# Optimization experiments

Measured on AMD Instinct MI355X. Metric: run time of the kernel, lower is better.

## Reference

```python
import jax, jax.numpy as jnp
import numpy as np

DT = 0.01        # base_dt from __init__
DT_SCALE = 1.0   # forward default


def setup_inputs() -> dict:
    key = jax.random.key(0)
    k1, k2, k3, k4, k5 = jax.random.split(key, 5)
    B, D, R = 4096, 512, 128
    x = jax.random.normal(k1, (B, D), dtype=jnp.float32)
    v = jax.random.normal(k2, (B, D), dtype=jnp.float32)
    force = jax.random.normal(k3, (B, D), dtype=jnp.float32)
    U = jax.random.normal(k4, (D, R), dtype=jnp.float32) * (1.0 / np.sqrt(D))
    W = jax.random.normal(k5, (R, D), dtype=jnp.float32) * (1.0 / np.sqrt(R))
    return {"x": x, "v": v, "force": force, "U": U, "W": W, "steps": 8}


def reference(x, v, force, U, W, steps):
    dt = DT * DT_SCALE
    # Dormand-Prince (DP5) tableau
    a21 = 1/5
    a31, a32 = 3/40, 9/40
    a41, a42, a43 = 44/45, -56/15, 32/9
    a51, a52, a53, a54 = 19372/6561, -25360/2187, 64448/6561, -212/729
    a61, a62, a63, a64, a65 = 9017/3168, -355/33, 46732/5247, 49/176, -5103/18656
    b1, b3, b4, b5, b6 = 35/384, 500/1113, 125/192, -2187/6784, 11/84

    def dynamics(tx, tv):
        # low-rank Christoffel: gamma(v, x) = ((v @ U) * (x @ U)) @ W
        acc = -jnp.einsum('br,rd->bd', (tv @ U) * (tx @ U), W)
        return acc + force

    def step(carry, _):
        cx, cv = carry
        k1x = cv
        k1v = dynamics(cx, cv)
        x2 = cx + dt * (a21 * k1x); v2 = cv + dt * (a21 * k1v)
        k2x = v2; k2v = dynamics(x2, v2)
        x3 = cx + dt * (a31 * k1x + a32 * k2x)
        v3 = cv + dt * (a31 * k1v + a32 * k2v)
        k3x = v3; k3v = dynamics(x3, v3)
        x4 = cx + dt * (a41 * k1x + a42 * k2x + a43 * k3x)
        v4 = cv + dt * (a41 * k1v + a42 * k2v + a43 * k3v)
        k4x = v4; k4v = dynamics(x4, v4)
        x5 = cx + dt * (a51 * k1x + a52 * k2x + a53 * k3x + a54 * k4x)
        v5 = cv + dt * (a51 * k1v + a52 * k2v + a53 * k3v + a54 * k4v)
        k5x = v5; k5v = dynamics(x5, v5)
        x6 = cx + dt * (a61 * k1x + a62 * k2x + a63 * k3x + a64 * k4x + a65 * k5x)
        v6 = cv + dt * (a61 * k1v + a62 * k2v + a63 * k3v + a64 * k4v + a65 * k5v)
        k6x = v6; k6v = dynamics(x6, v6)
        nx = cx + dt * (b1 * k1x + b3 * k3x + b4 * k4x + b5 * k5x + b6 * k6x)
        nv = cv + dt * (b1 * k1v + b3 * k3v + b4 * k4v + b5 * k5v + b6 * k6v)
        return (nx, nv), None

    (fx, fv), _ = jax.lax.scan(step, (x, v), None, length=steps)
    return fx, fv
```

## Files before the change

kernel.cpp:

```cpp
#include <hip/hip_runtime.h>


typedef _Float16 v8h __attribute__((ext_vector_type(8)));
typedef float v4f __attribute__((ext_vector_type(4)));
typedef unsigned short u16;
typedef unsigned int u32;

#define MFMAH __builtin_amdgcn_mfma_f32_16x16x32_f16
#define INV2048 4.8828125e-4f
#define INV256  0.00390625f
#define SSTR 144

__device__ __forceinline__ float swap8(float x){
  return __int_as_float(
    __builtin_amdgcn_mov_dpp(__float_as_int(x), 0x128, 0xf, 0xf, true));
}

struct Tab {
  double a[7][7]; double b[7]; double A[7]; double XC[7][7]; double XF[7]; double cxc[7];
};
static constexpr Tab make_tab() {
  Tab t{};
  t.a[2][1]=1.0/5;
  t.a[3][1]=3.0/40;       t.a[3][2]=9.0/40;
  t.a[4][1]=44.0/45;      t.a[4][2]=-56.0/15;      t.a[4][3]=32.0/9;
  t.a[5][1]=19372.0/6561; t.a[5][2]=-25360.0/2187; t.a[5][3]=64448.0/6561; t.a[5][4]=-212.0/729;
  t.a[6][1]=9017.0/3168;  t.a[6][2]=-355.0/33;     t.a[6][3]=46732.0/5247; t.a[6][4]=49.0/176; t.a[6][5]=-5103.0/18656;
  t.b[1]=35.0/384; t.b[2]=0.0; t.b[3]=500.0/1113; t.b[4]=125.0/192; t.b[5]=-2187.0/6784; t.b[6]=11.0/84;
  for (int i=1;i<=6;++i){ double s=0; for(int j=1;j<i;++j) s+=t.a[i][j]; t.A[i]=s; }
  for (int i=1;i<=6;++i) for(int l=1;l<i;++l){ double s=0; for(int j=l+1;j<i;++j) s+=t.a[i][j]*t.a[j][l]; t.XC[i][l]=s; }
  for (int i=1;i<=6;++i){ double s=0; for(int j=1;j<i;++j) s+=t.a[i][j]*t.A[j]; t.XF[i]=s; }
  for (int j=1;j<=6;++j){ double s=0; for (int i=j+1;i<=6;++i) s+=t.b[i]*t.a[i][j]; t.cxc[j]=s; }
  return t;
}
static constexpr Tab TB = make_tab();

__device__ __forceinline__ int decode_steps(const void* p){
  int v = *(const int*)p;
  if (v >= 1 && v <= 512) return v;
  float f = *(const float*)p;
  if (f >= 1.f && f <= 512.f) return (int)f;
  return 8;
}
__device__ __forceinline__ void split2s(float x, _Float16& h, _Float16& l){
  h = (_Float16)x;
  l = (_Float16)((x - (float)h) * 2048.0f);
}

#define WS_GH 0
#define WS_GL 16384
#define WS_UH 32768
#define WS_UL 98304
#define WS_WH 163840
#define WS_WL 229376

__global__ __launch_bounds__(512) void k_prep(const float* __restrict__ Ug,
                                              const float* __restrict__ Wg,
                                              _Float16* __restrict__ ws){
  const int tid = threadIdx.x;
  if (blockIdx.x >= 8) {
    int t = (blockIdx.x - 8)*512 + tid;
    if (t < 65536) {
      int r = t >> 7, c = t & 127;
      _Float16 h, l; split2s(Ug[t]*256.f, h, l);
      int kb=r>>5, q2=(r>>3)&3, j=r&7, n2=c>>4, cl=c&15;
      int slot = ((n2*16+kb)*64 + q2*16+cl)*8 + j;
      ws[WS_UH + slot] = h; ws[WS_UL + slot] = l;
    } else {
      int idx = t - 65536;
      int r = idx >> 9, c = idx & 511;
      _Float16 h, l; split2s(Wg[idx]*256.f, h, l);
      int kb=r>>5, q2=(r>>3)&3, j=r&7, n2=c>>4, cl=c&15;
      int slot = ((n2*4+kb)*64 + q2*16+cl)*8 + j;
      ws[WS_WH + slot] = h; ws[WS_WL + slot] = l;
    }
  } else {
    const int b = blockIdx.x;
    const int ww = tid >> 6, lane = tid & 63, q = lane >> 4, c16 = lane & 15;
    const int nb = ww;
    v4f aH = {0,0,0,0}, aC0 = {0,0,0,0}, aC1 = {0,0,0,0};
    #pragma unroll
    for (int kb = 0; kb < 16; ++kb) {
      const float* wp = Wg + (b*16 + c16)*512 + kb*32 + q*8;
      float4 w0 = *(const float4*)wp;
      float4 w1 = *(const float4*)(wp + 4);
      float wv[8] = {w0.x,w0.y,w0.z,w0.w, w1.x,w1.y,w1.z,w1.w};
      v8h Ah, Al, Bh, Bl;
      #pragma unroll
      for (int j = 0; j < 8; ++j) {
        _Float16 h, l; split2s(-wv[j], h, l);
        Ah[j] = h; Al[j] = l;
        float uv = Ug[(kb*32 + q*8 + j)*128 + nb*16 + c16] * 256.f;
        split2s(uv, h, l);
        Bh[j] = h; Bl[j] = l;
      }
      aH = MFMAH(Ah, Bh, aH, 0,0,0);
      if (kb & 1) {
        aC1 = MFMAH(Ah, Bl, aC1, 0,0,0);
        aC1 = MFMAH(Al, Bh, aC1, 0,0,0);
      } else {
        aC0 = MFMAH(Ah, Bl, aC0, 0,0,0);
        aC0 = MFMAH(Al, Bh, aC0, 0,0,0);
      }
    }
    #pragma unroll
    for (int r = 0; r < 4; ++r) {
      float g = aH[r] + (aC0[r] + aC1[r])*INV2048;
      _Float16 h, l; split2s(g, h, l);
      int m = b*16 + 4*q + r, n = nb*16 + c16;
      int slot = (((n>>4)*4 + (m>>5))*64 + ((m>>3)&3)*16 + (n&15))*8 + (m&7);
      ws[WS_GH + slot] = h; ws[WS_GL + slot] = l;
    }
  }
}

#define ARENA 49920

__global__ __launch_bounds__(512,4) void dp5_main(
    const float* __restrict__ xg, const float* __restrict__ vg,
    const float* __restrict__ fg, const void* stepsp,
    const _Float16* __restrict__ ws, float* __restrict__ outg)
{
  __shared__ __align__(16) char arena[ARENA];
  _Float16* base = (_Float16*)arena;
  const _Float16* uH = ws + WS_UH;
  const _Float16* uL = ws + WS_UL;
  const _Float16* wH = ws + WS_WH;
  const _Float16* wL = ws + WS_WL;

  const int tid  = threadIdx.x;
  const int ww   = tid >> 6;
  const int lane = tid & 63;
  const int q    = lane >> 4;
  const int c16  = lane & 15;
  const int nb   = ww;
  const int kcol = nb*16 + c16;
  const int srcl = (q>>1)*16 + c16;
  const bool odd = (q & 1);
  const int rb   = blockIdx.x * 8;
  const int S    = decode_steps(stepsp);
  const float dt = 0.01f;
  const int  brow = c16 & 7;
  const bool hiC  = (c16 >= 8);
  const int  kc0  = nb*16 + 4*q + (hiC ? 2 : 0);

  v8h Gh[4], Gl[4];
  #pragma unroll
  for (int kb = 0; kb < 4; ++kb) {
    int off = ((nb*4 + kb)*64 + lane)*8;
    Gh[kb] = *(const v8h*)(ws + WS_GH + off);
    Gl[kb] = *(const v8h*)(ws + WS_GL + off);
  }

  _Float16* tH = base;
  _Float16* tL = base + 12480;
  const int r16 = tid >> 5, c0 = (tid & 31)*16;
  float xU0[2], vU0[2], fU0[2];
  {
    {
      const float* sp = (r16 < 8) ? (xg + (rb + r16)*512) : (vg + (rb + r16 - 8)*512);
      sp += c0;
      float4 g0 = *(const float4*)(sp);
      float4 g1 = *(const float4*)(sp + 4);
      float4 g2 = *(const float4*)(sp + 8);
      float4 g3 = *(const float4*)(sp + 12);
      float vals[16] = {g0.x,g0.y,g0.z,g0.w, g1.x,g1.y,g1.z,g1.w,
                        g2.x,g2.y,g2.z,g2.w, g3.x,g3.y,g3.z,g3.w};
      v8h vh0, vh1, vl0, vl1;
      #pragma unroll
      for (int j = 0; j < 8; ++j) {
        _Float16 h, l;
        split2s(vals[j], h, l);     vh0[j] = h; vl0[j] = l;
        split2s(vals[8+j], h, l);   vh1[j] = h; vl1[j] = l;
      }
      int o = r16*520 + c0;
      *(v8h*)(tH + o) = vh0; *(v8h*)(tH + o + 8) = vh1;
      *(v8h*)(tL + o) = vl0; *(v8h*)(tL + o + 8) = vl1;
    }
    if (r16 < 8) {
      const float* sp = fg + (rb + r16)*512 + c0;
      float4 g0 = *(const float4*)(sp);
      float4 g1 = *(const float4*)(sp + 4);
      float4 g2 = *(const float4*)(sp + 8);
      float4 g3 = *(const float4*)(sp + 12);
      float vals[16] = {g0.x,g0.y,g0.z,g0.w, g1.x,g1.y,g1.z,g1.w,
                        g2.x,g2.y,g2.z,g2.w, g3.x,g3.y,g3.z,g3.w};
      v8h vh0, vh1, vl0, vl1;
      #pragma unroll
      for (int j = 0; j < 8; ++j) {
        _Float16 h, l;
        split2s(vals[j], h, l);     vh0[j] = h; vl0[j] = l;
        split2s(vals[8+j], h, l);   vh1[j] = h; vl1[j] = l;
      }
      int o = (16 + r16)*520 + c0;
      *(v8h*)(tH + o) = vh0; *(v8h*)(tH + o + 8) = vh1;
      *(v8h*)(tL + o) = vl0; *(v8h*)(tL + o + 8) = vl1;
    }
    __syncthreads();

    v4f aH0={0,0,0,0}, aH1={0,0,0,0}, aC0={0,0,0,0}, aC1={0,0,0,0};
    v4f bH0={0,0,0,0}, bH1={0,0,0,0}, bC0={0,0,0,0}, bC1={0,0,0,0};
    const int arow1 = (c16 < 8) ? (16 + c16) : c16;
    #pragma unroll
    for (int kb = 0; kb < 16; ++kb) {
      int ao0 = c16*520 + kb*32 + q*8;
      int ao1 = arow1*520 + kb*32 + q*8;
      v8h Ah0 = *(const v8h*)(tH + ao0);
      v8h Al0 = *(const v8h*)(tL + ao0);
      v8h Ah1 = *(const v8h*)(tH + ao1);
      v8h Al1 = *(const v8h*)(tL + ao1);
      int bo = ((nb*16 + kb)*64 + lane)*8;
      v8h Bh = *(const v8h*)(uH + bo);
      v8h Bl = *(const v8h*)(uL + bo);
      if (kb & 1) {
        aH1 = MFMAH(Ah0, Bh, aH1, 0,0,0);
        aC1 = MFMAH(Ah0, Bl, aC1, 0,0,0);
        aC1 = MFMAH(Al0, Bh, aC1, 0,0,0);
        bH1 = MFMAH(Ah1, Bh, bH1, 0,0,0);
        bC1 = MFMAH(Ah1, Bl, bC1, 0,0,0);
        bC1 = MFMAH(Al1, Bh, bC1, 0,0,0);
      } else {
        aH0 = MFMAH(Ah0, Bh, aH0, 0,0,0);
        aC0 = MFMAH(Ah0, Bl, aC0, 0,0,0);
        aC0 = MFMAH(Al0, Bh, aC0, 0,0,0);
        bH0 = MFMAH(Ah1, Bh, bH0, 0,0,0);
        bC0 = MFMAH(Ah1, Bl, bC0, 0,0,0);
        bC0 = MFMAH(Al1, Bh, bC0, 0,0,0);
      }
    }
    float at0 = ((aH0[0]+aH1[0]) + (aC0[0]+aC1[0])*INV2048)*INV256;
    float at1 = ((aH0[1]+aH1[1]) + (aC0[1]+aC1[1])*INV2048)*INV256;
    float at2 = ((aH0[2]+aH1[2]) + (aC0[2]+aC1[2])*INV2048)*INV256;
    float at3 = ((aH0[3]+aH1[3]) + (aC0[3]+aC1[3])*INV2048)*INV256;
    float bt0 = ((bH0[0]+bH1[0]) + (bC0[0]+bC1[0])*INV2048)*INV256;
    float bt1 = ((bH0[1]+bH1[1]) + (bC0[1]+bC1[1])*INV2048)*INV256;
    float bt2 = ((bH0[2]+bH1[2]) + (bC0[2]+bC1[2])*INV2048)*INV256;
    float bt3 = ((bH0[3]+bH1[3]) + (bC0[3]+bC1[3])*INV2048)*INV256;
    {
      float sx0=__shfl(at0,srcl,64), sx1=__shfl(at1,srcl,64);
      float sx2=__shfl(at2,srcl,64), sx3=__shfl(at3,srcl,64);
      xU0[0] = odd ? sx2 : sx0; xU0[1] = odd ? sx3 : sx1;
      int srclv = srcl + 32;
      float sv0=__shfl(at0,srclv,64), sv1=__shfl(at1,srclv,64);
      float sv2=__shfl(at2,srclv,64), sv3=__shfl(at3,srclv,64);
      vU0[0] = odd ? sv2 : sv0; vU0[1] = odd ? sv3 : sv1;
    }
    {
      float sf0=__shfl(bt0,srcl,64), sf1=__shfl(bt1,srcl,64);
      float sf2=__shfl(bt2,srcl,64), sf3=__shfl(bt3,srcl,64);
      fU0[0] = odd ? sf2 : sf0; fU0[1] = odd ? sf3 : sf1;
    }
    __syncthreads();
  }

  float cxU2[2], cvU2[2], fU2[2];
  {
    float* T = (float*)arena;
    #pragma unroll
    for (int p2 = 0; p2 < 3; ++p2) {
      float i0 = (p2==0) ? xU0[0] : (p2==1) ? vU0[0] : fU0[0];
      float i1 = (p2==0) ? xU0[1] : (p2==1) ? vU0[1] : fU0[1];
      T[(2*q + 0)*132 + kcol] = i0;
      T[(2*q + 1)*132 + kcol] = i1;
      __syncthreads();
      float2 t2 = *(const float2*)(T + brow*132 + kc0);
      float* o = (p2==0) ? cxU2 : (p2==1) ? cvU2 : fU2;
      o[0] = t2.x; o[1] = t2.y;
      __syncthreads();
    }
  }

  float kU6[6][2], Rr2[2], QXa2[2];
  #pragma unroll
  for (int j = 0; j < 2; ++j) {
    Rr2[j] = 0.f; QXa2[j] = 0.f;
    #pragma unroll
    for (int l = 0; l < 6; ++l) kU6[l][j] = 0.f;
  }

  int pb = 0;
  for (int s = 0; s < S; ++s) {
    float accX[2], accV[2], Pbs[2], Pxcs[2];
    #pragma unroll
    for (int j = 0; j < 2; ++j) { accX[j]=0.f; accV[j]=0.f; Pbs[j]=0.f; Pxcs[j]=0.f; }

    #pragma unroll
    for (int i = 1; i <= 6; ++i) {
      _Float16* bT = base + (pb ? 2304 : 0);
      const float dtA   = dt*(float)TB.A[i];
      const float dt2XF = dt*dt*(float)TB.XF[i];
      const float bi    = (float)TB.b[i];
      const float ci    = (float)TB.cxc[i];
      {
        union { _Float16 h[2]; u32 u; } ph, pl;
        #pragma unroll
        for (int j2 = 0; j2 < 2; ++j2) {
          float vv = cvU2[j2] + dtA*fU2[j2];
          float xx = cxU2[j2] + dtA*cvU2[j2] + dt2XF*fU2[j2];
          #pragma unroll
          for (int l = 1; l < i; ++l) {
            vv += (dt*(float)TB.a[i][l]) * kU6[l-1][j2];
            xx += (dt*dt*(float)TB.XC[i][l]) * kU6[l-1][j2];
          }
          float p = vv*xx;
          Pbs[j2] += bi*p; Pxcs[j2] += ci*p;
          _Float16 h, l2; split2s(p, h, l2);
          ph.h[j2] = h; pl.h[j2] = l2;
        }
        *(u32*)(bT + brow*SSTR + kc0)       = ph.u;
        *(u32*)(bT + (8+brow)*SSTR + kc0)   = pl.u;
      }
      __syncthreads();
      const _Float16* bp = bT + c16*SSTR + q*8;
      v8h B0 = *(const v8h*)(bp);
      v8h B1 = *(const v8h*)(bp + 32);
      v8h B2 = *(const v8h*)(bp + 64);
      v8h B3 = *(const v8h*)(bp + 96);
      v4f C1 = {0,0,0,0}, C2 = {0,0,0,0};
      C1 = MFMAH(Gh[0], B0, C1, 0,0,0);  C2 = MFMAH(Gl[0], B0, C2, 0,0,0);
      C1 = MFMAH(Gh[1], B1, C1, 0,0,0);  C2 = MFMAH(Gl[1], B1, C2, 0,0,0);
      C1 = MFMAH(Gh[2], B2, C1, 0,0,0);  C2 = MFMAH(Gl[2], B2, C2, 0,0,0);
      C1 = MFMAH(Gh[3], B3, C1, 0,0,0);  C2 = MFMAH(Gl[3], B3, C2, 0,0,0);
      float kv[4];
      #pragma unroll
      for (int r = 0; r < 4; ++r) {
        float oth = swap8(C1[r]);
        kv[r] = (C1[r] + (oth + C2[r])*INV2048)*INV256;
      }
      float k2 = swap8(kv[2]);
      float k3 = swap8(kv[3]);
      float kva = hiC ? k2 : kv[0];
      float kvb = hiC ? k3 : kv[1];
      kU6[i-1][0] = kva; kU6[i-1][1] = kvb;
      accX[0] += ci*kva; accV[0] += bi*kva;
      accX[1] += ci*kvb; accV[1] += bi*kvb;
      pb ^= 1;
    }

    #pragma unroll
    for (int j = 0; j < 2; ++j) {
      float nx = cxU2[j] + dt*cvU2[j] + dt*dt*(accX[j] + 0.5f*fU2[j]);
      cvU2[j] += dt*(accV[j] + fU2[j]);
      cxU2[j]  = nx;
      QXa2[j] += Rr2[j] + Pxcs[j];
      Rr2[j]  += Pbs[j];
    }
  }

  __syncthreads();
  _Float16* RQh = base;
  _Float16* RQl = base + 2176;
  {
    union { _Float16 h[2]; u32 u; } t1, t2, t3, t4;
    #pragma unroll
    for (int j2 = 0; j2 < 2; ++j2) {
      _Float16 h, l;
      split2s(Rr2[j2], h, l);  t1.h[j2] = h; t2.h[j2] = l;
      split2s(QXa2[j2], h, l); t3.h[j2] = h; t4.h[j2] = l;
    }
    *(u32*)(RQh + brow*136 + kc0)     = t1.u;
    *(u32*)(RQl + brow*136 + kc0)     = t2.u;
    *(u32*)(RQh + (8+brow)*136 + kc0) = t3.u;
    *(u32*)(RQl + (8+brow)*136 + kc0) = t4.u;
  }
  __syncthreads();

  float* axs = (float*)(arena + 9216);
  float* abs_ = (float*)(arena + 25600);

  #pragma unroll
  for (int cbi = 0; cbi < 4; ++cbi) {
    int cb = nb*4 + cbi;
    v4f aH={0,0,0,0}, aC0={0,0,0,0}, aC1={0,0,0,0};
    #pragma unroll
    for (int kb = 0; kb < 4; ++kb) {
      int bo = ((cb*4 + kb)*64 + lane)*8;
      v8h Bh = *(const v8h*)(wH + bo);
      v8h Bl = *(const v8h*)(wL + bo);
      int ao = c16*136 + kb*32 + q*8;
      v8h Ah = *(const v8h*)(RQh + ao);
      v8h Al = *(const v8h*)(RQl + ao);
      aH = MFMAH(Ah, Bh, aH, 0,0,0);
      if (kb & 1) {
        aC1 = MFMAH(Ah, Bl, aC1, 0,0,0);
        aC1 = MFMAH(Al, Bh, aC1, 0,0,0);
      } else {
        aC0 = MFMAH(Ah, Bl, aC0, 0,0,0);
        aC0 = MFMAH(Al, Bh, aC0, 0,0,0);
      }
    }
    float r0 = (aH[0] + (aC0[0]+aC1[0])*INV2048)*INV256;
    float r1 = (aH[1] + (aC0[1]+aC1[1])*INV2048)*INV256;
    float r2 = (aH[2] + (aC0[2]+aC1[2])*INV2048)*INV256;
    float r3 = (aH[3] + (aC0[3]+aC1[3])*INV2048)*INV256;
    float o0 = __shfl_xor(r0, 32, 64);
    float o1 = __shfl_xor(r1, 32, 64);
    float o2 = __shfl_xor(r2, 32, 64);
    float o3 = __shfl_xor(r3, 32, 64);
    if (q < 2) {
      float abv[4] = {r0, r1, r2, r3};
      float axv[4] = {o0, o1, o2, o3};
      #pragma unroll
      for (int i4 = 0; i4 < 4; ++i4) {
        int lrow = 4*q + i4;
        int lcol = cb*16 + c16;
        axs[lrow*512 + lcol]  = axv[i4];
        abs_[lrow*512 + lcol] = abv[i4];
      }
    }
  }
  __syncthreads();

  const float Sdt = (float)S * dt;
  #pragma unroll
  for (int half = 0; half < 2; ++half) {
    int flat = half*2048 + tid*4;
    int row  = flat >> 9;
    int col  = flat & 511;
    int go   = (rb + row)*512 + col;
    float4 xv = *(const float4*)(xg + go);
    float4 vv = *(const float4*)(vg + go);
    float4 fv = *(const float4*)(fg + go);
    float4 axf = *(const float4*)(axs + flat);
    float4 abf = *(const float4*)(abs_ + flat);
    float4 o1, o2;
    o1.x = xv.x + Sdt*vv.x + 0.5f*Sdt*Sdt*fv.x - dt*dt*axf.x;
    o1.y = xv.y + Sdt*vv.y + 0.5f*Sdt*Sdt*fv.y - dt*dt*axf.y;
    o1.z = xv.z + Sdt*vv.z + 0.5f*Sdt*Sdt*fv.z - dt*dt*axf.z;
    o1.w = xv.w + Sdt*vv.w + 0.5f*Sdt*Sdt*fv.w - dt*dt*axf.w;
    o2.x = vv.x + Sdt*fv.x - dt*abf.x;
    o2.y = vv.y + Sdt*fv.y - dt*abf.y;
    o2.z = vv.z + Sdt*fv.z - dt*abf.z;
    o2.w = vv.w + Sdt*fv.w - dt*abf.w;
    *(float4*)(outg + go) = o1;
    *(float4*)(outg + 2097152 + go) = o2;
  }
}

extern "C" void kernel_launch(void* const* d_in, const int* in_sizes, int n_in,
                              void* d_out, int out_size, void* d_ws, size_t ws_size,
                              hipStream_t stream) {
  const float* x = (const float*)d_in[0];
  const float* v = (const float*)d_in[1];
  const float* f = (const float*)d_in[2];
  const float* U = (const float*)d_in[3];
  const float* W = (const float*)d_in[4];
  _Float16* ws = (_Float16*)d_ws;

  k_prep<<<dim3(264), dim3(512), 0, stream>>>(U, W, ws);
  dp5_main<<<dim3(512), dim3(512), 0, stream>>>(
      x, v, f, d_in[5], ws, (float*)d_out);
}
```

Before: 136.4 us.

## Process two 8-row batches per block to interleave independent MFMA chains

Each block now handles 16 rows as two independent 8-row groups, A and B. Their per-stage phase-1 writes, MFMA chains and k-value extraction are interleaved so the two groups hide each other's latency and share the G fragments and barriers. The grid is halved and launch bounds are relaxed to 2 blocks per CU, which allows more registers but lowers occupancy. The projection and epilogue run twice per block. The k-value extraction is also reordered so the swaps apply to the selected lanes.

```diff
diff --git a/kernel.cpp b/kernel.cpp
--- a/kernel.cpp
+++ b/kernel.cpp
@@ -116,7 +116,7 @@
 
 #define ARENA 49920
 
-__global__ __launch_bounds__(512,4) void dp5_main(
+__global__ __launch_bounds__(512,2) void dp5_main(
     const float* __restrict__ xg, const float* __restrict__ vg,
     const float* __restrict__ fg, const void* stepsp,
     const _Float16* __restrict__ ws, float* __restrict__ outg)
@@ -137,26 +137,20 @@
   const int kcol = nb*16 + c16;
   const int srcl = (q>>1)*16 + c16;
   const bool odd = (q & 1);
-  const int rb   = blockIdx.x * 8;
+  const int rbA  = blockIdx.x * 16;
+  const int rbB  = rbA + 8;
   const int S    = decode_steps(stepsp);
   const float dt = 0.01f;
   const int  brow = c16 & 7;
   const bool hiC  = (c16 >= 8);
   const int  kc0  = nb*16 + 4*q + (hiC ? 2 : 0);
 
-  v8h Gh[4], Gl[4];
-  #pragma unroll
-  for (int kb = 0; kb < 4; ++kb) {
-    int off = ((nb*4 + kb)*64 + lane)*8;
-    Gh[kb] = *(const v8h*)(ws + WS_GH + off);
-    Gl[kb] = *(const v8h*)(ws + WS_GL + off);
-  }
-
-  _Float16* tH = base;
-  _Float16* tL = base + 12480;
   const int r16 = tid >> 5, c0 = (tid & 31)*16;
-  float xU0[2], vU0[2], fU0[2];
-  {
+
+  auto projection = [&](int rb, float cxU2[2], float cvU2[2], float fU2[2]) {
+    _Float16* tH = base;
+    _Float16* tL = base + 12480;
+    float xU0[2], vU0[2], fU0[2];
     {
       const float* sp = (r16 < 8) ? (xg + (rb + r16)*512) : (vg + (rb + r16 - 8)*512);
       sp += c0;
@@ -236,25 +230,24 @@
     float bt1 = ((bH0[1]+bH1[1]) + (bC0[1]+bC1[1])*INV2048)*INV256;
     float bt2 = ((bH0[2]+bH1[2]) + (bC0[2]+bC1[2])*INV2048)*INV256;
     float bt3 = ((bH0[3]+bH1[3]) + (bC0[3]+bC1[3])*INV2048)*INV256;
+    float xU0a, xU0b, vU0a, vU0b, fU0a, fU0b;
     {
       float sx0=__shfl(at0,srcl,64), sx1=__shfl(at1,srcl,64);
       float sx2=__shfl(at2,srcl,64), sx3=__shfl(at3,srcl,64);
-      xU0[0] = odd ? sx2 : sx0; xU0[1] = odd ? sx3 : sx1;
+      xU0a = odd ? sx2 : sx0; xU0b = odd ? sx3 : sx1;
       int srclv = srcl + 32;
       float sv0=__shfl(at0,srclv,64), sv1=__shfl(at1,srclv,64);
       float sv2=__shfl(at2,srclv,64), sv3=__shfl(at3,srclv,64);
-      vU0[0] = odd ? sv2 : sv0; vU0[1] = odd ? sv3 : sv1;
+      vU0a = odd ? sv2 : sv0; vU0b = odd ? sv3 : sv1;
     }
     {
       float sf0=__shfl(bt0,srcl,64), sf1=__shfl(bt1,srcl,64);
       float sf2=__shfl(bt2,srcl,64), sf3=__shfl(bt3,srcl,64);
-      fU0[0] = odd ? sf2 : sf0; fU0[1] = odd ? sf3 : sf1;
-    }
+      fU0a = odd ? sf2 : sf0; fU0b = odd ? sf3 : sf1;
+    }
+    xU0[0]=xU0a; xU0[1]=xU0b; vU0[0]=vU0a; vU0[1]=vU0b; fU0[0]=fU0a; fU0[1]=fU0b;
     __syncthreads();
-  }
-
-  float cxU2[2], cvU2[2], fU2[2];
-  {
+
     float* T = (float*)arena;
     #pragma unroll
     for (int p2 = 0; p2 < 3; ++p2) {
@@ -268,39 +261,59 @@
       o[0] = t2.x; o[1] = t2.y;
       __syncthreads();
     }
+  };
+
+  float cxA[2], cvA[2], fA[2], cxB[2], cvB[2], fB[2];
+  projection(rbA, cxA, cvA, fA);
+  projection(rbB, cxB, cvB, fB);
+
+  v8h Gh[4], Gl[4];
+  #pragma unroll
+  for (int kb = 0; kb < 4; ++kb) {
+    int off = ((nb*4 + kb)*64 + lane)*8;
+    Gh[kb] = *(const v8h*)(ws + WS_GH + off);
+    Gl[kb] = *(const v8h*)(ws + WS_GL + off);
   }
 
-  float kU6[6][2], Rr2[2], QXa2[2];
+  float kUA[6][2], kUB[6][2], RrA[2], RrB[2], QXA[2], QXB[2];
   #pragma unroll
   for (int j = 0; j < 2; ++j) {
-    Rr2[j] = 0.f; QXa2[j] = 0.f;
-    #pragma unroll
-    for (int l = 0; l < 6; ++l) kU6[l][j] = 0.f;
+    RrA[j]=0.f; RrB[j]=0.f; QXA[j]=0.f; QXB[j]=0.f;
+    #pragma unroll
+    for (int l = 0; l < 6; ++l) { kUA[l][j]=0.f; kUB[l][j]=0.f; }
   }
 
   int pb = 0;
   for (int s = 0; s < S; ++s) {
-    float accX[2], accV[2], Pbs[2], Pxcs[2];
-    #pragma unroll
-    for (int j = 0; j < 2; ++j) { accX[j]=0.f; accV[j]=0.f; Pbs[j]=0.f; Pxcs[j]=0.f; }
+    float accXA[2], accVA[2], PbsA[2], PxcsA[2];
+    float accXB[2], accVB[2], PbsB[2], PxcsB[2];
+    #pragma unroll
+    for (int j = 0; j < 2; ++j) {
+      accXA[j]=0.f; accVA[j]=0.f; PbsA[j]=0.f; PxcsA[j]=0.f;
+      accXB[j]=0.f; accVB[j]=0.f; PbsB[j]=0.f; PxcsB[j]=0.f;
+    }
 
     #pragma unroll
     for (int i = 1; i <= 6; ++i) {
-      _Float16* bT = base + (pb ? 2304 : 0);
+      _Float16* bTA = base + (pb ? 2304 : 0);
+      _Float16* bTB = base + 4608 + (pb ? 2304 : 0);
       const float dtA   = dt*(float)TB.A[i];
       const float dt2XF = dt*dt*(float)TB.XF[i];
       const float bi    = (float)TB.b[i];
       const float ci    = (float)TB.cxc[i];
-      {
+
+      auto phase1 = [&](_Float16* bT, const float cx[2], const float cv[2],
+                        const float ff[2], const float (*kU)[2],
+                        float Pbs[2], float Pxcs[2]) {
         union { _Float16 h[2]; u32 u; } ph, pl;
         #pragma unroll
         for (int j2 = 0; j2 < 2; ++j2) {
-          float vv = cvU2[j2] + dtA*fU2[j2];
-          float xx = cxU2[j2] + dtA*cvU2[j2] + dt2XF*fU2[j2];
+          float vv = cv[j2] + dtA*ff[j2];
+          float xx = cx[j2] + dtA*cv[j2] + dt2XF*ff[j2];
           #pragma unroll
           for (int l = 1; l < i; ++l) {
-            vv += (dt*(float)TB.a[i][l]) * kU6[l-1][j2];
-            xx += (dt*dt*(float)TB.XC[i][l]) * kU6[l-1][j2];
+            vv += (dt*(float)TB.a[i][l]) * kU[l-1][j2];
+            xx += (dt*dt*(float)TB.XC[i][l]) * kU[l-1][j2];
           }
           float p = vv*xx;
           Pbs[j2] += bi*p; Pxcs[j2] += ci*p;
@@ -309,132 +322,171 @@
         }
         *(u32*)(bT + brow*SSTR + kc0)       = ph.u;
         *(u32*)(bT + (8+brow)*SSTR + kc0)   = pl.u;
-      }
+      };
+      phase1(bTA, cxA, cvA, fA, kUA, PbsA, PxcsA);
+      phase1(bTB, cxB, cvB, fB, kUB, PbsB, PxcsB);
       __syncthreads();
-      const _Float16* bp = bT + c16*SSTR + q*8;
-      v8h B0 = *(const v8h*)(bp);
-      v8h B1 = *(const v8h*)(bp + 32);
-      v8h B2 = *(const v8h*)(bp + 64);
-      v8h B3 = *(const v8h*)(bp + 96);
-      v4f C1 = {0,0,0,0}, C2 = {0,0,0,0};
-      C1 = MFMAH(Gh[0], B0, C1, 0,0,0);  C2 = MFMAH(Gl[0], B0, C2, 0,0,0);
-      C1 = MFMAH(Gh[1], B1, C1, 0,0,0);  C2 = MFMAH(Gl[1], B1, C2, 0,0,0);
-      C1 = MFMAH(Gh[2], B2, C1, 0,0,0);  C2 = MFMAH(Gl[2], B2, C2, 0,0,0);
-      C1 = MFMAH(Gh[3], B3, C1, 0,0,0);  C2 = MFMAH(Gl[3], B3, C2, 0,0,0);
-      float kv[4];
+
+      const _Float16* bpA = bTA + c16*SSTR + q*8;
+      const _Float16* bpB = bTB + c16*SSTR + q*8;
+      v8h A0 = *(const v8h*)(bpA);
+      v8h A1 = *(const v8h*)(bpA + 32);
+      v8h A2 = *(const v8h*)(bpA + 64);
+      v8h A3 = *(const v8h*)(bpA + 96);
+      v8h Bb0 = *(const v8h*)(bpB);
+      v8h Bb1 = *(const v8h*)(bpB + 32);
+      v8h Bb2 = *(const v8h*)(bpB + 64);
+      v8h Bb3 = *(const v8h*)(bpB + 96);
+      v4f C1 = {0,0,0,0}, C2 = {0,0,0,0}, D1 = {0,0,0,0}, D2 = {0,0,0,0};
+      C1 = MFMAH(Gh[0], A0,  C1, 0,0,0);  D1 = MFMAH(Gh[0], Bb0, D1, 0,0,0);
+      C2 = MFMAH(Gl[0], A0,  C2, 0,0,0);  D2 = MFMAH(Gl[0], Bb0, D2, 0,0,0);
+      C1 = MFMAH(Gh[1], A1,  C1, 0,0,0);  D1 = MFMAH(Gh[1], Bb1, D1, 0,0,0);
+      C2 = MFMAH(Gl[1], A1,  C2, 0,0,0);  D2 = MFMAH(Gl[1], Bb1, D2, 0,0,0);
+      C1 = MFMAH(Gh[2], A2,  C1, 0,0,0);  D1 = MFMAH(Gh[2], Bb2, D1, 0,0,0);
+      C2 = MFMAH(Gl[2], A2,  C2, 0,0,0);  D2 = MFMAH(Gl[2], Bb2, D2, 0,0,0);
+      C1 = MFMAH(Gh[3], A3,  C1, 0,0,0);  D1 = MFMAH(Gh[3], Bb3, D1, 0,0,0);
+      C2 = MFMAH(Gl[3], A3,  C2, 0,0,0);  D2 = MFMAH(Gl[3], Bb3, D2, 0,0,0);
+
+      {
+        float sa0 = swap8(C1[0]), sa2 = swap8(C1[2]), sc2 = swap8(C2[2]);
+        float sb1 = swap8(C1[1]), sb3 = swap8(C1[3]), sd3 = swap8(C2[3]);
+        float m_a = hiC ? sa2   : C1[0];
+        float n_a = hiC ? C1[2] : sa0;
+        float c_a = hiC ? sc2   : C2[0];
+        float m_b = hiC ? sb3   : C1[1];
+        float n_b = hiC ? C1[3] : sb1;
+        float c_b = hiC ? sd3   : C2[1];
+        float kva = (m_a + (n_a + c_a)*INV2048)*INV256;
+        float kvb = (m_b + (n_b + c_b)*INV2048)*INV256;
+        kUA[i-1][0] = kva; kUA[i-1][1] = kvb;
+        accXA[0] += ci*kva; accVA[0] += bi*kva;
+        accXA[1] += ci*kvb; accVA[1] += bi*kvb;
+      }
+      {
+        float sa0 = swap8(D1[0]), sa2 = swap8(D1[2]), sc2 = swap8(D2[2]);
+        float sb1 = swap8(D1[1]), sb3 = swap8(D1[3]), sd3 = swap8(D2[3]);
+        float m_a = hiC ? sa2   : D1[0];
+        float n_a = hiC ? D1[2] : sa0;
+        float c_a = hiC ? sc2   : D2[0];
+        float m_b = hiC ? sb3   : D1[1];
+        float n_b = hiC ? D1[3] : sb1;
+        float c_b = hiC ? sd3   : D2[1];
+        float kva = (m_a + (n_a + c_a)*INV2048)*INV256;
+        float kvb = (m_b + (n_b + c_b)*INV2048)*INV256;
+        kUB[i-1][0] = kva; kUB[i-1][1] = kvb;
+        accXB[0] += ci*kva; accVB[0] += bi*kva;
+        accXB[1] += ci*kvb; accVB[1] += bi*kvb;
+      }
+      pb ^= 1;
+    }
+
+    #pragma unroll
+    for (int j = 0; j < 2; ++j) {
+      float nxA = cxA[j] + dt*cvA[j] + dt*dt*(accXA[j] + 0.5f*fA[j]);
+      cvA[j] += dt*(accVA[j] + fA[j]);
+      cxA[j]  = nxA;
+      QXA[j] += RrA[j] + PxcsA[j];
+      RrA[j] += PbsA[j];
+      float nxB = cxB[j] + dt*cvB[j] + dt*dt*(accXB[j] + 0.5f*fB[j]);
+      cvB[j] += dt*(accVB[j] + fB[j]);
+      cxB[j]  = nxB;
+      QXB[j] += RrB[j] + PxcsB[j];
+      RrB[j] += PbsB[j];
+    }
+  }
+
+  const float Sdt = (float)S * dt;
+  auto epilogue = [&](int rb, const float Rr2[2], const float QXa2[2]) {
+    __syncthreads();
+    _Float16* RQh = base;
+    _Float16* RQl = base + 2176;
+    {
+      union { _Float16 h[2]; u32 u; } t1, t2, t3, t4;
       #pragma unroll
-      for (int r = 0; r < 4; ++r) {
-        float oth = swap8(C1[r]);
-        kv[r] = (C1[r] + (oth + C2[r])*INV2048)*INV256;
-      }
-      float k2 = swap8(kv[2]);
-      float k3 = swap8(kv[3]);
-      float kva = hiC ? k2 : kv[0];
-      float kvb = hiC ? k3 : kv[1];
-      kU6[i-1][0] = kva; kU6[i-1][1] = kvb;
-      accX[0] += ci*kva; accV[0] += bi*kva;
-      accX[1] += ci*kvb; accV[1] += bi*kvb;
-      pb ^= 1;
-    }
-
-    #pragma unroll
-    for (int j = 0; j < 2; ++j) {
-      float nx = cxU2[j] + dt*cvU2[j] + dt*dt*(accX[j] + 0.5f*fU2[j]);
-      cvU2[j] += dt*(accV[j] + fU2[j]);
-      cxU2[j]  = nx;
-      QXa2[j] += Rr2[j] + Pxcs[j];
-      Rr2[j]  += Pbs[j];
-    }
-  }
-
-  __syncthreads();
-  _Float16* RQh = base;
-  _Float16* RQl = base + 2176;
-  {
-    union { _Float16 h[2]; u32 u; } t1, t2, t3, t4;
-    #pragma unroll
-    for (int j2 = 0; j2 < 2; ++j2) {
-      _Float16 h, l;
-      split2s(Rr2[j2], h, l);  t1.h[j2] = h; t2.h[j2] = l;
-      split2s(QXa2[j2], h, l); t3.h[j2] = h; t4.h[j2] = l;
-    }
-    *(u32*)(RQh + brow*136 + kc0)     = t1.u;
-    *(u32*)(RQl + brow*136 + kc0)     = t2.u;
-    *(u32*)(RQh + (8+brow)*136 + kc0) = t3.u;
-    *(u32*)(RQl + (8+brow)*136 + kc0) = t4.u;
-  }
-  __syncthreads();
-
-  float* axs = (float*)(arena + 9216);
-  float* abs_ = (float*)(arena + 25600);
-
-  #pragma unroll
-  for (int cbi = 0; cbi < 4; ++cbi) {
-    int cb = nb*4 + cbi;
-    v4f aH={0,0,0,0}, aC0={0,0,0,0}, aC1={0,0,0,0};
-    #pragma unroll
-    for (int kb = 0; kb < 4; ++kb) {
-      int bo = ((cb*4 + kb)*64 + lane)*8;
-      v8h Bh = *(const v8h*)(wH + bo);
-      v8h Bl = *(const v8h*)(wL + bo);
-      int ao = c16*136 + kb*32 + q*8;
-      v8h Ah = *(const v8h*)(RQh + ao);
-      v8h Al = *(const v8h*)(RQl + ao);
-      aH = MFMAH(Ah, Bh, aH, 0,0,0);
-      if (kb & 1) {
-        aC1 = MFMAH(Ah, Bl, aC1, 0,0,0);
-        aC1 = MFMAH(Al, Bh, aC1, 0,0,0);
-      } else {
-        aC0 = MFMAH(Ah, Bl, aC0, 0,0,0);
-        aC0 = MFMAH(Al, Bh, aC0, 0,0,0);
-      }
-    }
-    float r0 = (aH[0] + (aC0[0]+aC1[0])*INV2048)*INV256;
-    float r1 = (aH[1] + (aC0[1]+aC1[1])*INV2048)*INV256;
-    float r2 = (aH[2] + (aC0[2]+aC1[2])*INV2048)*INV256;
-    float r3 = (aH[3] + (aC0[3]+aC1[3])*INV2048)*INV256;
-    float o0 = __shfl_xor(r0, 32, 64);
-    float o1 = __shfl_xor(r1, 32, 64);
-    float o2 = __shfl_xor(r2, 32, 64);
-    float o3 = __shfl_xor(r3, 32, 64);
-    if (q < 2) {
-      float abv[4] = {r0, r1, r2, r3};
-      float axv[4] = {o0, o1, o2, o3};
+      for (int j2 = 0; j2 < 2; ++j2) {
+        _Float16 h, l;
+        split2s(Rr2[j2], h, l);  t1.h[j2] = h; t2.h[j2] = l;
+        split2s(QXa2[j2], h, l); t3.h[j2] = h; t4.h[j2] = l;
+      }
+      *(u32*)(RQh + brow*136 + kc0)     = t1.u;
+      *(u32*)(RQl + brow*136 + kc0)     = t2.u;
+      *(u32*)(RQh + (8+brow)*136 + kc0) = t3.u;
+      *(u32*)(RQl + (8+brow)*136 + kc0) = t4.u;
+    }
+    __syncthreads();
+
+    float* axs  = (float*)(arena + 9216);
+    float* abs_ = (float*)(arena + 25600);
+
+    #pragma unroll
+    for (int cbi = 0; cbi < 4; ++cbi) {
+      int cb = nb*4 + cbi;
+      v4f aH={0,0,0,0}, aC0={0,0,0,0}, aC1={0,0,0,0};
       #pragma unroll
-      for (int i4 = 0; i4 < 4; ++i4) {
-        int lrow = 4*q + i4;
-        int lcol = cb*16 + c16;
-        axs[lrow*512 + lcol]  = axv[i4];
-        abs_[lrow*512 + lcol] = abv[i4];
-      }
-    }
-  }
-  __syncthreads();
-
-  const float Sdt = (float)S * dt;
-  #pragma unroll
-  for (int half = 0; half < 2; ++half) {
-    int flat = half*2048 + tid*4;
-    int row  = flat >> 9;
-    int col  = flat & 511;
-    int go   = (rb + row)*512 + col;
-    float4 xv = *(const float4*)(xg + go);
-    float4 vv = *(const float4*)(vg + go);
-    float4 fv = *(const float4*)(fg + go);
-    float4 axf = *(const float4*)(axs + flat);
-    float4 abf = *(const float4*)(abs_ + flat);
-    float4 o1, o2;
-    o1.x = xv.x + Sdt*vv.x + 0.5f*Sdt*Sdt*fv.x - dt*dt*axf.x;
-    o1.y = xv.y + Sdt*vv.y + 0.5f*Sdt*Sdt*fv.y - dt*dt*axf.y;
-    o1.z = xv.z + Sdt*vv.z + 0.5f*Sdt*Sdt*fv.z - dt*dt*axf.z;
-    o1.w = xv.w + Sdt*vv.w + 0.5f*Sdt*Sdt*fv.w - dt*dt*axf.w;
-    o2.x = vv.x + Sdt*fv.x - dt*abf.x;
-    o2.y = vv.y + Sdt*fv.y - dt*abf.y;
-    o2.z = vv.z + Sdt*fv.z - dt*abf.z;
-    o2.w = vv.w + Sdt*fv.w - dt*abf.w;
-    *(float4*)(outg + go) = o1;
-    *(float4*)(outg + 2097152 + go) = o2;
-  }
+      for (int kb = 0; kb < 4; ++kb) {
+        int bo = ((cb*4 + kb)*64 + lane)*8;
+        v8h Bh = *(const v8h*)(wH + bo);
+        v8h Bl = *(const v8h*)(wL + bo);
+        int ao = c16*136 + kb*32 + q*8;
+        v8h Ah = *(const v8h*)(RQh + ao);
+        v8h Al = *(const v8h*)(RQl + ao);
+        aH = MFMAH(Ah, Bh, aH, 0,0,0);
+        if (kb & 1) {
+          aC1 = MFMAH(Ah, Bl, aC1, 0,0,0);
+          aC1 = MFMAH(Al, Bh, aC1, 0,0,0);
+        } else {
+          aC0 = MFMAH(Ah, Bl, aC0, 0,0,0);
+          aC0 = MFMAH(Al, Bh, aC0, 0,0,0);
+        }
+      }
+      float r0 = (aH[0] + (aC0[0]+aC1[0])*INV2048)*INV256;
+      float r1 = (aH[1] + (aC0[1]+aC1[1])*INV2048)*INV256;
+      float r2 = (aH[2] + (aC0[2]+aC1[2])*INV2048)*INV256;
+      float r3 = (aH[3] + (aC0[3]+aC1[3])*INV2048)*INV256;
+      float o0 = __shfl_xor(r0, 32, 64);
+      float o1 = __shfl_xor(r1, 32, 64);
+      float o2 = __shfl_xor(r2, 32, 64);
+      float o3 = __shfl_xor(r3, 32, 64);
+      if (q < 2) {
+        float abv[4] = {r0, r1, r2, r3};
+        float axv[4] = {o0, o1, o2, o3};
+        #pragma unroll
+        for (int i4 = 0; i4 < 4; ++i4) {
+          int lrow = 4*q + i4;
+          int lcol = cb*16 + c16;
+          axs[lrow*512 + lcol]  = axv[i4];
+          abs_[lrow*512 + lcol] = abv[i4];
+        }
+      }
+    }
+    __syncthreads();
+
+    #pragma unroll
+    for (int half = 0; half < 2; ++half) {
+      int flat = half*2048 + tid*4;
+      int row  = flat >> 9;
+      int col  = flat & 511;
+      int go   = (rb + row)*512 + col;
+      float4 xv = *(const float4*)(xg + go);
+      float4 vv = *(const float4*)(vg + go);
+      float4 fv = *(const float4*)(fg + go);
+      float4 axf = *(const float4*)(axs + flat);
+      float4 abf = *(const float4*)(abs_ + flat);
+      float4 o1, o2;
+      o1.x = xv.x + Sdt*vv.x + 0.5f*Sdt*Sdt*fv.x - dt*dt*axf.x;
+      o1.y = xv.y + Sdt*vv.y + 0.5f*Sdt*Sdt*fv.y - dt*dt*axf.y;
+      o1.z = xv.z + Sdt*vv.z + 0.5f*Sdt*Sdt*fv.z - dt*dt*axf.z;
+      o1.w = xv.w + Sdt*vv.w + 0.5f*Sdt*Sdt*fv.w - dt*dt*axf.w;
+      o2.x = vv.x + Sdt*fv.x - dt*abf.x;
+      o2.y = vv.y + Sdt*fv.y - dt*abf.y;
+      o2.z = vv.z + Sdt*fv.z - dt*abf.z;
+      o2.w = vv.w + Sdt*fv.w - dt*abf.w;
+      *(float4*)(outg + go) = o1;
+      *(float4*)(outg + 2097152 + go) = o2;
+    }
+  };
+  epilogue(rbA, RrA, QXA);
+  epilogue(rbB, RrB, QXB);
 }
 
 extern "C" void kernel_launch(void* const* d_in, const int* in_sizes, int n_in,
@@ -448,6 +500,6 @@
   _Float16* ws = (_Float16*)d_ws;
 
   k_prep<<<dim3(264), dim3(512), 0, stream>>>(U, W, ws);
-  dp5_main<<<dim3(512), dim3(512), 0, stream>>>(
+  dp5_main<<<dim3(256), dim3(512), 0, stream>>>(
       x, v, f, d_in[5], ws, (float*)d_out);
 }
```

Measured after the change: 147.2 us. 7.9% more time.
